# Kernel tuning notes

Hardware: AMD Instinct MI355X
Metric: run time of the kernel (lower is better)

Reference implementation:

```python
import jax, jax.numpy as jnp
import numpy as np

N, E, F_IN, H, C = 50000, 800000, 64, 4, 32
NEG_SLOPE = 0.2  # PyG GATConv default negative_slope
LN_EPS = 1e-5


def setup_inputs() -> dict:
    key = jax.random.key(0)
    ks = jax.random.split(key, 8)
    s = 1.0 / np.sqrt(F_IN)
    return {
        "x": jax.random.normal(ks[0], (N, F_IN), jnp.float32),
        "edge_index": jax.random.randint(ks[1], (2, E), 0, N, jnp.int64),
        "W": jax.random.normal(ks[2], (F_IN, H * C), jnp.float32) * s,
        "att_src": jax.random.normal(ks[3], (H, C), jnp.float32) * s,
        "att_dst": jax.random.normal(ks[4], (H, C), jnp.float32) * s,
        "bias": jnp.zeros((H * C,), jnp.float32),
        "res_w": jax.random.normal(ks[5], (F_IN, H * C), jnp.float32) * s,
        "res_b": jnp.zeros((H * C,), jnp.float32),
        "ln_g": jnp.ones((H * C,), jnp.float32),
        "ln_b": jnp.zeros((H * C,), jnp.float32),
    }


def reference(x, edge_index, W, att_src, att_dst, bias, res_w, res_b, ln_g, ln_b):
    n = x.shape[0]
    # GATConv adds self-loops by default
    loop = jnp.arange(n, dtype=edge_index.dtype)
    src = jnp.concatenate([edge_index[0], loop])
    dst = jnp.concatenate([edge_index[1], loop])

    h = (x @ W).reshape(n, H, C)                      # [N,H,C]
    a_src = jnp.einsum('nhc,hc->nh', h, att_src)       # [N,H]
    a_dst = jnp.einsum('nhc,hc->nh', h, att_dst)

    e = a_src[src] + a_dst[dst]                        # [Etot,H]
    e = jnp.where(e >= 0, e, NEG_SLOPE * e)            # leaky_relu

    # segment softmax over destination nodes
    m = jax.ops.segment_max(e, dst, num_segments=n)    # [N,H]
    ex = jnp.exp(e - m[dst])
    denom = jax.ops.segment_sum(ex, dst, num_segments=n)
    alpha = ex / denom[dst]                            # [Etot,H]

    msg = h[src] * alpha[:, :, None]                   # [Etot,H,C]
    out = jax.ops.segment_sum(msg, dst, num_segments=n)  # [N,H,C]
    out = out.reshape(n, H * C) + bias

    # elu; dropout is identity in eval mode
    out = jnp.where(out > 0, out, jnp.expm1(out))
    out = out + (x @ res_w + res_b)                    # residual Linear

    mu = out.mean(-1, keepdims=True)
    var = ((out - mu) ** 2).mean(-1, keepdims=True)
    return ln_g * (out - mu) * jax.lax.rsqrt(var + LN_EPS) + ln_b
```

## Files before the change

kernel.cpp:

```cpp
#include <hip/hip_runtime.h>

#define F_IN 64
#define NH 4
#define HC 128
#define NEG_SLOPE 0.2f
#define LN_EPS 1e-5f
#define BUCKET 128
#define BKT_CAP 2560
#define NSC 128
#define CCAP 44
#define KREG 25
#define KW_BLOCKS 64

typedef __bf16 bf16_8 __attribute__((ext_vector_type(8)));
typedef float  f32_4  __attribute__((ext_vector_type(4)));

__device__ inline int detect_is64(const int* __restrict__ ei, int E) {
    int lane = threadIdx.x & 63;
    long long stride = (2LL * E) / 65;
    int w = ei[(((long long)(lane + 1)) * stride) | 1];
    return __ballot(w != 0) == 0ULL;
}

__device__ inline unsigned bfpack(float a, float b) {
    unsigned ua = __float_as_uint(a), ub = __float_as_uint(b);
    ua = (ua + 0x7fffu + ((ua >> 16) & 1u)) >> 16;
    ub = (ub + 0x7fffu + ((ub >> 16) & 1u)) >> 16;
    return ua | (ub << 16);
}

__global__ __launch_bounds__(256) void k_pre(
    const float* __restrict__ W, const float* __restrict__ res_w,
    __bf16* __restrict__ wt,
    const int* __restrict__ ei, int E,
    int* __restrict__ counts, unsigned* __restrict__ epk, int chunk, int NB)
{
    if ((int)blockIdx.x >= NSC) {
        int idx = (blockIdx.x - NSC) * 256 + threadIdx.x;
        int ch = idx >> 6, k = idx & 63;
        const float* src = (ch < HC) ? W : res_w;
        wt[ch * 64 + k] = (__bf16)src[k * HC + (ch & (HC - 1))];
        return;
    }

    __shared__ int bcur[512];
    int c = blockIdx.x, t = threadIdx.x;
    for (int i = t; i < NB; i += 256) bcur[i] = 0;
    __syncthreads();
    int is64 = detect_is64(ei, E);
    int base = c * chunk, end = min(E, base + chunk);

    unsigned rg[KREG];
#pragma unroll
    for (int i = 0; i < KREG; ++i) {
        int idx = base + i * 256 + t;
        unsigned ent = 0xFFFFFFFFu;
        if (idx < end) {
            int s = is64 ? ei[2 * idx] : ei[idx];
            int d = is64 ? ei[2 * (E + idx)] : ei[E + idx];
            ent = ((unsigned)d << 16) | (unsigned)s;
            atomicAdd(&bcur[d >> 7], 1);
        }
        rg[i] = ent;
    }
    __syncthreads();

    for (int bb = t; bb < NB; bb += 256) {
        int f = bcur[bb]; if (f > CCAP) f = CCAP;
        counts[c * NB + bb] = f;
        bcur[bb] = 0;
    }
    __syncthreads();

#pragma unroll
    for (int i = 0; i < KREG; ++i) {
        unsigned ent = rg[i];
        if (ent != 0xFFFFFFFFu) {
            int bb = ent >> 23;
            int p = atomicAdd(&bcur[bb], 1);
            if (p < CCAP)
                epk[((size_t)c * NB + bb) * CCAP + p] = ent;
        }
    }
}

__global__ __launch_bounds__(256) void k_mid(
    const float* __restrict__ x, const __bf16* __restrict__ wt,
    const float* __restrict__ att_src, const float* __restrict__ att_dst,
    unsigned* __restrict__ h_bf, unsigned* __restrict__ r_bf,
    float* __restrict__ a_s, float* __restrict__ a_d, int n, int nka,
    const int* __restrict__ counts, const unsigned* __restrict__ epk,
    unsigned short* __restrict__ ssorted, unsigned* __restrict__ offdeg, int NB)
{
    __shared__ int cnt_s[NSC];
    __shared__ int hist[BUCKET], sc[BUCKET], cur[BUCKET];

    if ((int)blockIdx.x < nka) {
        int tid = threadIdx.x;
        int wv_ = tid >> 6, lane = tid & 63;
        int col = lane & 15, quad = lane >> 4;
        int node = blockIdx.x * 64 + wv_ * 16 + col;
        int nrow = (node < n) ? node : (n - 1);

        bf16_8 bx0, bx1;
        {
            const float* xp = &x[nrow * F_IN + quad * 8];
            float4 p0 = *(const float4*)(xp);
            float4 p1 = *(const float4*)(xp + 4);
            float4 p2 = *(const float4*)(xp + 32);
            float4 p3 = *(const float4*)(xp + 36);
            bx0[0] = (__bf16)p0.x; bx0[1] = (__bf16)p0.y; bx0[2] = (__bf16)p0.z; bx0[3] = (__bf16)p0.w;
            bx0[4] = (__bf16)p1.x; bx0[5] = (__bf16)p1.y; bx0[6] = (__bf16)p1.z; bx0[7] = (__bf16)p1.w;
            bx1[0] = (__bf16)p2.x; bx1[1] = (__bf16)p2.y; bx1[2] = (__bf16)p2.z; bx1[3] = (__bf16)p2.w;
            bx1[4] = (__bf16)p3.x; bx1[5] = (__bf16)p3.y; bx1[6] = (__bf16)p3.z; bx1[7] = (__bf16)p3.w;
        }

        float vs[4] = {0.f, 0.f, 0.f, 0.f};
        float vd[4] = {0.f, 0.f, 0.f, 0.f};

#pragma unroll
        for (int mt = 0; mt < 16; ++mt) {
            const __bf16* ap = &wt[(mt * 16 + col) * 64 + quad * 8];
            bf16_8 a0 = *(const bf16_8*)ap;
            bf16_8 a1 = *(const bf16_8*)(ap + 32);
            f32_4 acc = {0.f, 0.f, 0.f, 0.f};
            acc = __builtin_amdgcn_mfma_f32_16x16x32_bf16(a0, bx0, acc, 0, 0, 0);
            acc = __builtin_amdgcn_mfma_f32_16x16x32_bf16(a1, bx1, acc, 0, 0, 0);
            int ch0 = mt * 16 + quad * 4;
            if (mt < 8) {
                float4 as4 = *(const float4*)&att_src[ch0];
                float4 ad4 = *(const float4*)&att_dst[ch0];
                int head = mt >> 1;
                vs[head] += acc[0] * as4.x + acc[1] * as4.y + acc[2] * as4.z + acc[3] * as4.w;
                vd[head] += acc[0] * ad4.x + acc[1] * ad4.y + acc[2] * ad4.z + acc[3] * ad4.w;
                if (node < n) {
                    uint2 pk = make_uint2(bfpack(acc[0], acc[1]), bfpack(acc[2], acc[3]));
                    *(uint2*)&h_bf[node * 64 + (ch0 >> 1)] = pk;
                }
            } else {
                if (node < n) {
                    uint2 pk = make_uint2(bfpack(acc[0], acc[1]), bfpack(acc[2], acc[3]));
                    *(uint2*)&r_bf[node * 64 + ((ch0 - 128) >> 1)] = pk;
                }
            }
        }

#pragma unroll
        for (int hh = 0; hh < NH; ++hh) {
            vs[hh] += __shfl_down(vs[hh], 32, 64);
            vs[hh] += __shfl_down(vs[hh], 16, 64);
            vd[hh] += __shfl_down(vd[hh], 32, 64);
            vd[hh] += __shfl_down(vd[hh], 16, 64);
        }
        if (quad == 0 && node < n) {
            *(float4*)&a_s[node * NH] = make_float4(vs[0], vs[1], vs[2], vs[3]);
            *(float4*)&a_d[node * NH] = make_float4(vd[0], vd[1], vd[2], vd[3]);
        }
        return;
    }

    int b = blockIdx.x - nka, t = threadIdx.x;
    if (t < NSC) cnt_s[t] = counts[t * NB + b];
    if (t < BUCKET) hist[t] = 0;
    __syncthreads();

    for (int slot = t; slot < NSC * CCAP; slot += 256) {
        int c = slot / CCAP, j = slot - c * CCAP;
        if (j < cnt_s[c]) {
            unsigned ent = epk[((size_t)c * NB + b) * CCAP + j];
            atomicAdd(&hist[(ent >> 16) & (BUCKET - 1)], 1);
        }
    }
    __syncthreads();

    if (t < BUCKET) sc[t] = (hist[t] + 1) & ~1;
    __syncthreads();
#pragma unroll
    for (int o = 1; o < BUCKET; o <<= 1) {
        int u = (t >= o && t < BUCKET) ? sc[t - o] : 0;
        __syncthreads();
        if (t < BUCKET) sc[t] += u;
        __syncthreads();
    }
    if (t < BUCKET) {
        int excl = sc[t] - ((hist[t] + 1) & ~1);
        cur[t] = excl;
        int d = b * BUCKET + t;
        if (d < n)
            offdeg[d] = ((unsigned)(b * BKT_CAP + excl) << 12) | (unsigned)hist[t];
    }
    __syncthreads();

    unsigned short* outp = ssorted + (size_t)b * BKT_CAP;
    for (int slot = t; slot < NSC * CCAP; slot += 256) {
        int c = slot / CCAP, j = slot - c * CCAP;
        if (j < cnt_s[c]) {
            unsigned ent = epk[((size_t)c * NB + b) * CCAP + j];
            int p = atomicAdd(&cur[(ent >> 16) & (BUCKET - 1)], 1);
            if (p < BKT_CAP) outp[p] = (unsigned short)(ent & 0xffffu);
        }
    }
}

__global__ __launch_bounds__(256) void k_agg(
    const unsigned* __restrict__ offdeg, const unsigned short* __restrict__ ssorted,
    const float* __restrict__ a_s, const float* __restrict__ a_d,
    const unsigned int* __restrict__ h_bf, const unsigned int* __restrict__ r_bf,
    const float* __restrict__ bias, const float* __restrict__ res_b,
    const float* __restrict__ ln_g, const float* __restrict__ ln_b,
    float* __restrict__ out, int n)
{
    int wv = threadIdx.x >> 6, lane = threadIdx.x & 63;
    int d = blockIdx.x * 4 + wv;
    if (d >= n) return;
    int eh = lane >> 4;
    int g  = lane & 15;
    int head = g >> 2;
    float ad = a_d[d * NH + head];

    float ac[8] = {0.f, 0.f, 0.f, 0.f, 0.f, 0.f, 0.f, 0.f};
    float denom = 0.f;

#define ACCUM(WW, VV)                                                      \
    do {                                                                   \
        ac[0] += (WW) * __uint_as_float((VV).x << 16);                     \
        ac[1] += (WW) * __uint_as_float((VV).x & 0xffff0000u);             \
        ac[2] += (WW) * __uint_as_float((VV).y << 16);                     \
        ac[3] += (WW) * __uint_as_float((VV).y & 0xffff0000u);             \
        ac[4] += (WW) * __uint_as_float((VV).z << 16);                     \
        ac[5] += (WW) * __uint_as_float((VV).z & 0xffff0000u);             \
        ac[6] += (WW) * __uint_as_float((VV).w << 16);                     \
        ac[7] += (WW) * __uint_as_float((VV).w & 0xffff0000u);             \
    } while (0)

    {
        float e = a_s[d * NH + head] + ad;
        e = fmaxf(e, NEG_SLOPE * e);
        float w = (eh == 0) ? __expf(e) : 0.f;
        uint4 hv = *(const uint4*)&h_bf[d * 64 + 4 * g];
        ACCUM(w, hv);
        denom += w;
    }

    unsigned od = offdeg[d];
    int deg = od & 4095;
    const unsigned short* sl = &ssorted[od >> 12];
    int k = 0;
    if (k + 7 < deg) {
        unsigned sp = *(const unsigned*)&sl[k + 2 * eh];
        for (; k + 7 < deg; ) {
            int kn = k + 8;
            unsigned spn = 0;
            if (kn + 7 < deg)
                spn = *(const unsigned*)&sl[kn + 2 * eh];
            int s0 = sp & 0xffffu, s1 = sp >> 16;
            float e0 = a_s[s0 * NH + head];
            float e1 = a_s[s1 * NH + head];
            uint4 v0 = *(const uint4*)&h_bf[s0 * 64 + 4 * g];
            uint4 v1 = *(const uint4*)&h_bf[s1 * 64 + 4 * g];
            e0 += ad; e0 = fmaxf(e0, NEG_SLOPE * e0);
            float w0 = __expf(e0);
            e1 += ad; e1 = fmaxf(e1, NEG_SLOPE * e1);
            float w1 = __expf(e1);
            denom += w0 + w1;
            ACCUM(w0, v0);
            ACCUM(w1, v1);
            sp = spn; k = kn;
        }
    }
    for (; k < deg; k += 4) {
        int idx = k + eh;
        int valid = idx < deg;
        int s0 = valid ? sl[idx] : 0;
        float e0 = a_s[s0 * NH + head] + ad;
        uint4 v0 = *(const uint4*)&h_bf[s0 * 64 + 4 * g];
        e0 = fmaxf(e0, NEG_SLOPE * e0);
        float w0 = valid ? __expf(e0) : 0.f;
        denom += w0;
        ACCUM(w0, v0);
    }
#undef ACCUM

#pragma unroll
    for (int j = 0; j < 8; ++j) {
        ac[j] += __shfl_xor(ac[j], 32, 64);
        ac[j] += __shfl_xor(ac[j], 16, 64);
    }
    denom += __shfl_xor(denom, 32, 64);
    denom += __shfl_xor(denom, 16, 64);

    int c0 = g * 8;
    float4 bi0 = *(const float4*)&bias[c0];
    float4 bi1 = *(const float4*)&bias[c0 + 4];
    float4 rb0 = *(const float4*)&res_b[c0];
    float4 rb1 = *(const float4*)&res_b[c0 + 4];
    uint4 rv = *(const uint4*)&r_bf[d * 64 + 4 * g];

    float inv = 1.f / denom;
    float o[8];
    o[0] = ac[0] * inv + bi0.x; o[1] = ac[1] * inv + bi0.y;
    o[2] = ac[2] * inv + bi0.z; o[3] = ac[3] * inv + bi0.w;
    o[4] = ac[4] * inv + bi1.x; o[5] = ac[5] * inv + bi1.y;
    o[6] = ac[6] * inv + bi1.z; o[7] = ac[7] * inv + bi1.w;
#pragma unroll
    for (int j = 0; j < 8; ++j)
        o[j] = (o[j] > 0.f) ? o[j] : (__expf(o[j]) - 1.f);
    o[0] += __uint_as_float(rv.x << 16) + rb0.x;
    o[1] += __uint_as_float(rv.x & 0xffff0000u) + rb0.y;
    o[2] += __uint_as_float(rv.y << 16) + rb0.z;
    o[3] += __uint_as_float(rv.y & 0xffff0000u) + rb0.w;
    o[4] += __uint_as_float(rv.z << 16) + rb1.x;
    o[5] += __uint_as_float(rv.z & 0xffff0000u) + rb1.y;
    o[6] += __uint_as_float(rv.w << 16) + rb1.z;
    o[7] += __uint_as_float(rv.w & 0xffff0000u) + rb1.w;

    float ps = o[0] + o[1] + o[2] + o[3] + o[4] + o[5] + o[6] + o[7];
#pragma unroll
    for (int off = 32; off > 0; off >>= 1) ps += __shfl_down(ps, off, 64);
    float mean = __shfl(ps, 0, 64) * (1.f / (4 * HC));
    float dv[8], pv = 0.f;
#pragma unroll
    for (int j = 0; j < 8; ++j) { dv[j] = o[j] - mean; pv += dv[j] * dv[j]; }
#pragma unroll
    for (int off = 32; off > 0; off >>= 1) pv += __shfl_down(pv, off, 64);
    float var = __shfl(pv, 0, 64) * (1.f / (4 * HC));
    float rs = rsqrtf(var + LN_EPS);
    if (eh == 0) {
        float4 gg0 = *(const float4*)&ln_g[c0];
        float4 gg1 = *(const float4*)&ln_g[c0 + 4];
        float4 lb0 = *(const float4*)&ln_b[c0];
        float4 lb1 = *(const float4*)&ln_b[c0 + 4];
        *(float4*)&out[d * HC + c0] =
            make_float4(gg0.x * dv[0] * rs + lb0.x, gg0.y * dv[1] * rs + lb0.y,
                        gg0.z * dv[2] * rs + lb0.z, gg0.w * dv[3] * rs + lb0.w);
        *(float4*)&out[d * HC + c0 + 4] =
            make_float4(gg1.x * dv[4] * rs + lb1.x, gg1.y * dv[5] * rs + lb1.y,
                        gg1.z * dv[6] * rs + lb1.z, gg1.w * dv[7] * rs + lb1.w);
    }
}

extern "C" void kernel_launch(void* const* d_in, const int* in_sizes, int n_in,
                              void* d_out, int out_size, void* d_ws, size_t ws_size,
                              hipStream_t stream) {
    const float* x       = (const float*)d_in[0];
    const int*   ei      = (const int*)d_in[1];
    const float* W       = (const float*)d_in[2];
    const float* att_src = (const float*)d_in[3];
    const float* att_dst = (const float*)d_in[4];
    const float* bias    = (const float*)d_in[5];
    const float* res_w   = (const float*)d_in[6];
    const float* res_b   = (const float*)d_in[7];
    const float* ln_g    = (const float*)d_in[8];
    const float* ln_b    = (const float*)d_in[9];
    float* out = (float*)d_out;

    int n = in_sizes[0] / F_IN;
    int E = in_sizes[1] / 2;
    int NB = (n + BUCKET - 1) / BUCKET;
    int chunk = (E + NSC - 1) / NSC;
    int nka = (n + 63) / 64;

    unsigned*       h_bf   = (unsigned*)d_ws;
    unsigned*       r_bf   = h_bf + (size_t)n * 64;
    float*          a_s    = (float*)(r_bf + (size_t)n * 64);
    float*          a_d    = a_s + (size_t)n * NH;
    int*            counts = (int*)(a_d + (size_t)n * NH);
    unsigned*       epk    = (unsigned*)(counts + NSC * NB);
    unsigned short* ssd    = (unsigned short*)(epk + (size_t)NSC * NB * CCAP);
    unsigned*       offdeg = (unsigned*)(ssd + (size_t)NB * BKT_CAP);
    __bf16*         wt     = (__bf16*)(offdeg + n);

    k_pre<<<NSC + KW_BLOCKS, 256, 0, stream>>>(
        W, res_w, wt, ei, E, counts, epk, chunk, NB);

    k_mid<<<nka + NB, 256, 0, stream>>>(
        x, wt, att_src, att_dst, h_bf, r_bf, a_s, a_d, n, nka,
        counts, epk, ssd, offdeg, NB);

    k_agg<<<(n + 3) / 4, 256, 0, stream>>>(offdeg, ssd, a_s, a_d, h_bf, r_bf,
                                           bias, res_b, ln_g, ln_b, out, n);
}
```

Measured before the change: 173.1 us.

## Merge edge bucketing with projection GEMM and split the sort into its own kernel

The edge-bucketing scatter blocks and the node projection GEMM blocks now run in a single launch (k_main). Each GEMM block converts W and res_w to packed bf16 itself, so the GEMM no longer has to wait for a separate weight-conversion step. The per-bucket sort moves into its own kernel (kd_sort), which runs after the scatter finishes. In exchange, every GEMM block redundantly converts the full weight matrix and writes it to a shared global buffer, racing with the other blocks on identical values. That adds a lot of global write traffic and extra work per block.

```diff
diff --git a/kernel.cpp b/kernel.cpp
--- a/kernel.cpp
+++ b/kernel.cpp
@@ -10,7 +10,6 @@
 #define NSC 128
 #define CCAP 44
 #define KREG 25
-#define KW_BLOCKS 64
 
 typedef __bf16 bf16_8 __attribute__((ext_vector_type(8)));
 typedef float  f32_4  __attribute__((ext_vector_type(4)));
@@ -29,77 +28,37 @@
     return ua | (ub << 16);
 }
 
-__global__ __launch_bounds__(256) void k_pre(
-    const float* __restrict__ W, const float* __restrict__ res_w,
+__global__ __launch_bounds__(256) void k_main(
+    const float* __restrict__ x, const float* __restrict__ W,
+    const float* __restrict__ res_w,
+    const float* __restrict__ att_src, const float* __restrict__ att_dst,
     __bf16* __restrict__ wt,
+    unsigned* __restrict__ h_bf, unsigned* __restrict__ r_bf,
+    float* __restrict__ a_s, float* __restrict__ a_d, int n,
     const int* __restrict__ ei, int E,
     int* __restrict__ counts, unsigned* __restrict__ epk, int chunk, int NB)
 {
+    __shared__ int bcur[512];
+
     if ((int)blockIdx.x >= NSC) {
-        int idx = (blockIdx.x - NSC) * 256 + threadIdx.x;
-        int ch = idx >> 6, k = idx & 63;
-        const float* src = (ch < HC) ? W : res_w;
-        wt[ch * 64 + k] = (__bf16)src[k * HC + (ch & (HC - 1))];
-        return;
-    }
-
-    __shared__ int bcur[512];
-    int c = blockIdx.x, t = threadIdx.x;
-    for (int i = t; i < NB; i += 256) bcur[i] = 0;
-    __syncthreads();
-    int is64 = detect_is64(ei, E);
-    int base = c * chunk, end = min(E, base + chunk);
-
-    unsigned rg[KREG];
-#pragma unroll
-    for (int i = 0; i < KREG; ++i) {
-        int idx = base + i * 256 + t;
-        unsigned ent = 0xFFFFFFFFu;
-        if (idx < end) {
-            int s = is64 ? ei[2 * idx] : ei[idx];
-            int d = is64 ? ei[2 * (E + idx)] : ei[E + idx];
-            ent = ((unsigned)d << 16) | (unsigned)s;
-            atomicAdd(&bcur[d >> 7], 1);
-        }
-        rg[i] = ent;
-    }
-    __syncthreads();
-
-    for (int bb = t; bb < NB; bb += 256) {
-        int f = bcur[bb]; if (f > CCAP) f = CCAP;
-        counts[c * NB + bb] = f;
-        bcur[bb] = 0;
-    }
-    __syncthreads();
-
-#pragma unroll
-    for (int i = 0; i < KREG; ++i) {
-        unsigned ent = rg[i];
-        if (ent != 0xFFFFFFFFu) {
-            int bb = ent >> 23;
-            int p = atomicAdd(&bcur[bb], 1);
-            if (p < CCAP)
-                epk[((size_t)c * NB + bb) * CCAP + p] = ent;
-        }
-    }
-}
-
-__global__ __launch_bounds__(256) void k_mid(
-    const float* __restrict__ x, const __bf16* __restrict__ wt,
-    const float* __restrict__ att_src, const float* __restrict__ att_dst,
-    unsigned* __restrict__ h_bf, unsigned* __restrict__ r_bf,
-    float* __restrict__ a_s, float* __restrict__ a_d, int n, int nka,
-    const int* __restrict__ counts, const unsigned* __restrict__ epk,
-    unsigned short* __restrict__ ssorted, unsigned* __restrict__ offdeg, int NB)
-{
-    __shared__ int cnt_s[NSC];
-    __shared__ int hist[BUCKET], sc[BUCKET], cur[BUCKET];
-
-    if ((int)blockIdx.x < nka) {
         int tid = threadIdx.x;
+#pragma unroll
+        for (int jj = 0; jj < 32; ++jj) {
+            int idx = jj * 256 + tid;
+            int ch = idx >> 5;
+            int j5 = idx & 31;
+            int k0 = j5 * 2;
+            const float* src = (ch < HC) ? W : res_w;
+            int cc = ch & (HC - 1);
+            float lo = src[k0 * HC + cc];
+            float hi = src[(k0 + 1) * HC + cc];
+            ((unsigned*)wt)[ch * 32 + j5] = bfpack(lo, hi);
+        }
+        __syncthreads();
+
         int wv_ = tid >> 6, lane = tid & 63;
         int col = lane & 15, quad = lane >> 4;
-        int node = blockIdx.x * 64 + wv_ * 16 + col;
+        int node = (blockIdx.x - NSC) * 64 + wv_ * 16 + col;
         int nrow = (node < n) ? node : (n - 1);
 
         bf16_8 bx0, bx1;
@@ -159,7 +118,54 @@
         return;
     }
 
-    int b = blockIdx.x - nka, t = threadIdx.x;
+    int c = blockIdx.x, t = threadIdx.x;
+    for (int i = t; i < NB; i += 256) bcur[i] = 0;
+    __syncthreads();
+    int is64 = detect_is64(ei, E);
+    int base = c * chunk, end = min(E, base + chunk);
+
+    unsigned rg[KREG];
+#pragma unroll
+    for (int i = 0; i < KREG; ++i) {
+        int idx = base + i * 256 + t;
+        unsigned ent = 0xFFFFFFFFu;
+        if (idx < end) {
+            int s = is64 ? ei[2 * idx] : ei[idx];
+            int d = is64 ? ei[2 * (E + idx)] : ei[E + idx];
+            ent = ((unsigned)d << 16) | (unsigned)s;
+            atomicAdd(&bcur[d >> 7], 1);
+        }
+        rg[i] = ent;
+    }
+    __syncthreads();
+
+    for (int bb = t; bb < NB; bb += 256) {
+        int f = bcur[bb]; if (f > CCAP) f = CCAP;
+        counts[c * NB + bb] = f;
+        bcur[bb] = 0;
+    }
+    __syncthreads();
+
+#pragma unroll
+    for (int i = 0; i < KREG; ++i) {
+        unsigned ent = rg[i];
+        if (ent != 0xFFFFFFFFu) {
+            int bb = ent >> 23;
+            int p = atomicAdd(&bcur[bb], 1);
+            if (p < CCAP)
+                epk[((size_t)c * NB + bb) * CCAP + p] = ent;
+        }
+    }
+}
+
+__global__ __launch_bounds__(256) void kd_sort(
+    const int* __restrict__ counts, const unsigned* __restrict__ epk,
+    unsigned short* __restrict__ ssorted, unsigned* __restrict__ offdeg,
+    int n, int NB)
+{
+    __shared__ int cnt_s[NSC];
+    __shared__ int hist[BUCKET], sc[BUCKET], cur[BUCKET];
+    int b = blockIdx.x, t = threadIdx.x;
     if (t < NSC) cnt_s[t] = counts[t * NB + b];
     if (t < BUCKET) hist[t] = 0;
     __syncthreads();
@@ -370,12 +376,11 @@
     unsigned*       offdeg = (unsigned*)(ssd + (size_t)NB * BKT_CAP);
     __bf16*         wt     = (__bf16*)(offdeg + n);
 
-    k_pre<<<NSC + KW_BLOCKS, 256, 0, stream>>>(
-        W, res_w, wt, ei, E, counts, epk, chunk, NB);
-
-    k_mid<<<nka + NB, 256, 0, stream>>>(
-        x, wt, att_src, att_dst, h_bf, r_bf, a_s, a_d, n, nka,
-        counts, epk, ssd, offdeg, NB);
+    k_main<<<NSC + nka, 256, 0, stream>>>(
+        x, W, res_w, att_src, att_dst, wt, h_bf, r_bf, a_s, a_d, n,
+        ei, E, counts, epk, chunk, NB);
+
+    kd_sort<<<NB, 256, 0, stream>>>(counts, epk, ssd, offdeg, n, NB);
 
     k_agg<<<(n + 3) / 4, 256, 0, stream>>>(offdeg, ssd, a_s, a_d, h_bf, r_bf,
                                            bias, res_b, ln_g, ln_b, out, n);
```

New measurement: 193.1 us. 1.12x slower.
